# Kernel optimization log

Hardware: AMD Instinct MI355X
Metric: run time of the kernel (lower is better)

## Reference

```python
import jax, jax.numpy as jnp
import numpy as np

K = 16          # neighbors, matches init k
CHUNK = 2048    # query chunk size for kNN (avoids NxN dist matrix in one shot)


def knn_points(coords, k):
    """coords: (N,3). Returns squared dists (N,k) and indices (N,k), self included (dist 0)."""
    N = coords.shape[0]
    sq = jnp.sum(coords * coords, axis=-1)  # (N,)

    def chunk_fn(args):
        cq, cqs = args  # (CHUNK,3), (CHUNK,)
        # squared distance: |a|^2 + |b|^2 - 2 a.b  -> (CHUNK, N)
        d2 = cqs[:, None] + sq[None, :] - 2.0 * (cq @ coords.T)
        neg, idx = jax.lax.top_k(-d2, k)  # smallest distances
        return -neg, idx

    nchunks = N // CHUNK
    cc = coords.reshape(nchunks, CHUNK, 3)
    cs = sq.reshape(nchunks, CHUNK)
    d, i = jax.lax.map(chunk_fn, (cc, cs))
    return d.reshape(N, k), i.reshape(N, k)


def edge_conv_single(coords, feats, W1, b1, W2, b2):
    """One point cloud: coords (N,3), feats (N,C) -> (N,C)."""
    dists, idx = knn_points(coords, K)            # (N,k), (N,k)
    nn_feats = feats[idx]                         # (N,k,C) gather
    delta = nn_feats - feats[:, None, :]          # (N,k,C)
    grouped = jnp.concatenate([nn_feats, delta], axis=-1)  # (N,k,2C)
    h = jax.nn.relu(grouped @ W1 + b1)            # (N,k,inter)
    theta = h @ W2 + b2                           # (N,k,C)
    w = jax.nn.softmax(-dists, axis=1)            # (N,k) distance-softmax
    return jnp.einsum('nk,nkc->nc', w, theta)     # weighted average over neighbors


def setup_inputs() -> dict:
    key = jax.random.key(0)
    k1, k2, k3, k4 = jax.random.split(key, 4)
    B, N, C, INTER = 2, 16384, 256, 128
    coords = jax.random.uniform(k1, (B, N, 3), dtype=jnp.float32) * 100.0
    feats = jax.random.normal(k2, (B, N, C), dtype=jnp.float32)
    W1 = jax.random.normal(k3, (2 * C, INTER), dtype=jnp.float32) * 0.02
    b1 = jnp.zeros((INTER,), dtype=jnp.float32)
    W2 = jax.random.normal(k4, (INTER, C), dtype=jnp.float32) * 0.02
    b2 = jnp.zeros((C,), dtype=jnp.float32)
    return {"coords": coords, "feats": feats, "W1": W1, "b1": b1, "W2": W2, "b2": b2}


def reference(coords, feats, W1, b1, W2, b2):
    # batch loop in the original is embarrassingly parallel -> vmap over clouds
    return jax.vmap(edge_conv_single, in_axes=(0, 0, None, None, None, None))(
        coords, feats, W1, b1, W2, b2)
```

## Files before the change

kernel.cpp:

```cpp
#include <hip/hip_runtime.h>
#include <hip/hip_bf16.h>

#define NPTS   16384
#define NCLOUD 2
#define NTOT   (NPTS*NCLOUD)
#define CDIM   256
#define IDIM   128
#define KNN    16
#define GS     16
#define NCELL  (GS*GS*GS)
#define CELL_H 6.25f
#define INV_H  0.16f
#define SLABCAP 256

typedef __attribute__((ext_vector_type(8))) short s16x8;
typedef __attribute__((ext_vector_type(4))) float f32x4;

__device__ __forceinline__ int cell_coord(float v) {
    int c = (int)(v * INV_H);
    return c < 0 ? 0 : (c > GS-1 ? GS-1 : c);
}

__global__ __launch_bounds__(256) void prep_kernel(
        const float* __restrict__ W1, const float* __restrict__ W2,
        float* __restrict__ ABTf, float* __restrict__ W2Tf) {
    int i = blockIdx.x*256 + threadIdx.x;
    if (i < 65536) {
        int n = i >> 8, k = i & 255;
        float v = (n < IDIM) ? (W1[k*IDIM + n] + W1[(k+CDIM)*IDIM + n])
                             : W1[(k+CDIM)*IDIM + (n-IDIM)];
        ABTf[n*CDIM + k] = v;
    } else {
        int j = i - 65536;
        int n = j >> 7, k = j & 127;
        W2Tf[n*IDIM + k] = W2[k*CDIM + n];
    }
}

__global__ __launch_bounds__(256) void count_kernel(
        const float* __restrict__ coords, int* __restrict__ cnt) {
    int t = blockIdx.x * 256 + threadIdx.x;
    float x = coords[(size_t)t*3+0], y = coords[(size_t)t*3+1], z = coords[(size_t)t*3+2];
    int g = (t >> 14) * NCELL + (cell_coord(z)*GS + cell_coord(y))*GS + cell_coord(x);
    atomicAdd(&cnt[g], 1);
}

__global__ __launch_bounds__(1024) void scan_kernel(
        const int* __restrict__ cnt, int* __restrict__ cellstart,
        int* __restrict__ cursor) {
    __shared__ int sums[1024];
    const int tid = threadIdx.x;
    int local[8];
    int s = 0;
#pragma unroll
    for (int j = 0; j < 8; ++j) { local[j] = cnt[tid*8+j]; s += local[j]; }
    sums[tid] = s;
    __syncthreads();
    for (int off = 1; off < 1024; off <<= 1) {
        int v = (tid >= off) ? sums[tid-off] : 0;
        __syncthreads();
        sums[tid] += v;
        __syncthreads();
    }
    int run = sums[tid] - s;
#pragma unroll
    for (int j = 0; j < 8; ++j) {
        cellstart[tid*8+j] = run; cursor[tid*8+j] = run; run += local[j];
    }
    if (tid == 1023) cellstart[2*NCELL] = run;
}

__global__ __launch_bounds__(256) void scatter_kernel(
        const float* __restrict__ coords, int* __restrict__ cursor,
        float4* __restrict__ sorted, int* __restrict__ perm) {
    int t = blockIdx.x * 256 + threadIdx.x;
    float x = coords[(size_t)t*3+0], y = coords[(size_t)t*3+1], z = coords[(size_t)t*3+2];
    int g = (t >> 14) * NCELL + (cell_coord(z)*GS + cell_coord(y))*GS + cell_coord(x);
    int pos = atomicAdd(&cursor[g], 1);
    sorted[pos] = make_float4(x, y, z, __int_as_float(t));
    perm[pos] = t;
}

__device__ __forceinline__ void ring_off(int R, int s, int& dy, int& dz) {
    if (R == 0) { dy = 0; dz = 0; return; }
    int w = 2*R+1;
    if (s < w)        { dy = -R + s;       dz = -R; }
    else if (s < 2*w) { dy = -R + (s - w); dz =  R; }
    else {
        int rem = s - 2*w;
        if (rem < 2*R-1) { dy = -R; dz = -R+1+rem; }
        else             { dy =  R; dz = -R+1+(rem-(2*R-1)); }
    }
}

#define TOP16_INSERT(d2v, jjv) do {                                   \
    float _d2 = (d2v);                                                \
    if (_d2 < d[KNN-1]) {                                             \
        int _jj = (jjv); bool sa = true;                              \
        _Pragma("unroll")                                             \
        for (int s_ = KNN-1; s_ > 0; --s_) {                          \
            bool sh = _d2 < d[s_-1];                                  \
            float nd = sh ? d[s_-1] : (sa ? _d2 : d[s_]);             \
            int   ni = sh ? id[s_-1] : (sa ? _jj : id[s_]);           \
            d[s_] = nd; id[s_] = ni; sa = sh;                         \
        }                                                             \
        if (sa) { d[0] = _d2; id[0] = _jj; }                          \
    } } while (0)

__global__ __launch_bounds__(64) void knn_win_kernel(
        const float4* __restrict__ sorted, const int* __restrict__ cellstart,
        float* __restrict__ knn_d2, int* __restrict__ knn_idx) {
    __shared__ float ldsx[SLABCAP], ldsy[SLABCAP], ldsz[SLABCAP];
    __shared__ int cellofs[GS+1];
    const int t = threadIdx.x;
    const int bid = blockIdx.x;
    const int brow = bid >> 1, chunk = bid & 1;
    const int b  = brow >> 8;
    const int yz = brow & 255;
    const int cy = yz & 15, cz = yz >> 4;
    const int gq = b*NCELL + yz*16;
    const int qstart = cellstart[gq];
    const int qcount = cellstart[gq + GS] - qstart;

    for (int q0 = chunk*64; q0 < qcount; q0 += 64) {
        const bool active = (q0 + t < qcount);
        const float4 q = sorted[qstart + (active ? q0 + t : 0)];
        const int cx = cell_coord(q.x);
        const int wlo = cx-2 < 0 ? 0 : cx-2;
        const int whi = cx+2 > GS-1 ? GS-1 : cx+2;

        float d[KNN]; int id[KNN];
#pragma unroll
        for (int s = 0; s < KNN; ++s) { d[s] = 3.4e38f; id[s] = 0; }
        bool fin = !active;
        bool alldone = false;

        for (int phase = 0; phase < 2 && !alldone; ++phase) {
            for (int R = 0; R < GS && !alldone; ++R) {
                const int nseg = R ? 8*R : 1;
                for (int s = 0; s < nseg; ++s) {
                    int dy, dz;
                    ring_off(R, s, dy, dz);
                    const int yy = cy + dy, zz = cz + dz;
                    if (yy < 0 || yy > GS-1 || zz < 0 || zz > GS-1) continue;
                    const int g  = b*NCELL + (zz*GS + yy)*GS;
                    const int st = cellstart[g];
                    int n = cellstart[g + GS] - st;
                    if (n > SLABCAP) n = SLABCAP;
                    __syncthreads();
                    if (t < GS+1) {
                        int v = cellstart[g + t] - st;
                        cellofs[t] = v > n ? n : v;
                    }
                    for (int i = t; i < n; i += 64) {
                        float4 c = sorted[st + i];
                        ldsx[i] = c.x; ldsy[i] = c.y; ldsz[i] = c.z;
                    }
                    __syncthreads();
                    if (!fin) {
                        const int lo = cellofs[wlo], hi = cellofs[whi+1];
                        if (phase == 0) {
                            for (int e = lo; e < hi; ++e) {
                                float dx = q.x-ldsx[e], dy_ = q.y-ldsy[e], dz_ = q.z-ldsz[e];
                                TOP16_INSERT(dx*dx + dy_*dy_ + dz_*dz_, st + e);
                            }
                        } else {
                            for (int e = 0; e < n; ++e) {
                                if (e >= lo && e < hi) continue;
                                float dx = q.x-ldsx[e], dy_ = q.y-ldsy[e], dz_ = q.z-ldsz[e];
                                TOP16_INSERT(dx*dx + dy_*dy_ + dz_*dz_, st + e);
                            }
                        }
                    }
                }
                float bl = 1e30f;
                if (cy - R >= 1)    bl = fminf(bl, q.y - (float)(cy-R)*CELL_H);
                if (cy + R <= GS-2) bl = fminf(bl, (float)(cy+R+1)*CELL_H - q.y);
                if (cz - R >= 1)    bl = fminf(bl, q.z - (float)(cz-R)*CELL_H);
                if (cz + R <= GS-2) bl = fminf(bl, (float)(cz+R+1)*CELL_H - q.z);
                if (phase == 0) {
                    if (cx - 2 >= 1)    bl = fminf(bl, q.x - (float)(cx-2)*CELL_H);
                    if (cx + 2 <= GS-2) bl = fminf(bl, (float)(cx+3)*CELL_H - q.x);
                }
                fin = fin || (d[KNN-1] <= bl*bl);
                alldone = __syncthreads_and((int)fin);
            }
        }
        if (active) {
            const int o = qstart + q0 + t;
#pragma unroll
            for (int s = 0; s < KNN; ++s) {
                knn_d2 [(size_t)o*KNN + s] = d[s];
                knn_idx[(size_t)o*KNN + s] = id[s];
            }
        }
        if (chunk == 0) break;
    }
}

__device__ __forceinline__ void pack_split(float4 v, uint2& h, uint2& l) {
    __hip_bfloat16 h0=__float2bfloat16(v.x), h1=__float2bfloat16(v.y),
                   h2=__float2bfloat16(v.z), h3=__float2bfloat16(v.w);
    float r0=v.x-__bfloat162float(h0), r1=v.y-__bfloat162float(h1),
          r2=v.z-__bfloat162float(h2), r3=v.w-__bfloat162float(h3);
    __hip_bfloat16 l0=__float2bfloat16(r0), l1=__float2bfloat16(r1),
                   l2=__float2bfloat16(r2), l3=__float2bfloat16(r3);
    h.x = (unsigned)*(unsigned short*)&h0 | ((unsigned)*(unsigned short*)&h1 << 16);
    h.y = (unsigned)*(unsigned short*)&h2 | ((unsigned)*(unsigned short*)&h3 << 16);
    l.x = (unsigned)*(unsigned short*)&l0 | ((unsigned)*(unsigned short*)&l1 << 16);
    l.y = (unsigned)*(unsigned short*)&l2 | ((unsigned)*(unsigned short*)&l3 << 16);
}

template<int KDIM, bool BIAS, bool GATHER_A, bool SCATTER_OUT>
__global__ __launch_bounds__(256) void gemm_split_kernel(
        const float* __restrict__ A,
        const float* __restrict__ BT,
        const float* __restrict__ bias,
        const int*   __restrict__ permA,
        const int*   __restrict__ permOut,
        float* __restrict__ C_, int M, int N) {
    __shared__ unsigned short AsH[128*40], AsL[128*40], BsH[128*40], BsL[128*40];
    const int tid = threadIdx.x;
    const int l = tid & 63, w = tid >> 6;
    const int wm = w >> 1, wn = w & 1;
    const int bm = blockIdx.x * 128, bn = blockIdx.y * 128;
    const f32x4 zero = {0.f, 0.f, 0.f, 0.f};
    f32x4 acc[4][4];
#pragma unroll
    for (int m = 0; m < 4; ++m)
#pragma unroll
        for (int n = 0; n < 4; ++n) acc[m][n] = zero;

    for (int k0 = 0; k0 < KDIM; k0 += 32) {
        __syncthreads();
#pragma unroll
        for (int r2 = 0; r2 < 4; ++r2) {
            int flat = r2*256 + tid;
            int row = flat >> 3, ke = (flat & 7) * 4;
            int ga = bm + row;
            if (GATHER_A) ga = permA[ga];
            float4 va = *(const float4*)&A[(size_t)ga*KDIM + k0 + ke];
            uint2 uh, ul; pack_split(va, uh, ul);
            *(uint2*)&AsH[row*40 + ke] = uh;
            *(uint2*)&AsL[row*40 + ke] = ul;
            float4 vb = *(const float4*)&BT[(size_t)(bn + row)*KDIM + k0 + ke];
            uint2 vh, vl; pack_split(vb, vh, vl);
            *(uint2*)&BsH[row*40 + ke] = vh;
            *(uint2*)&BsL[row*40 + ke] = vl;
        }
        __syncthreads();
        s16x8 ah[4], al[4], bh[4], bl[4];
        const int ks = (l >> 4) * 8;
#pragma unroll
        for (int m = 0; m < 4; ++m) {
            int r = wm*64 + m*16 + (l & 15);
            ah[m] = *(const s16x8*)&AsH[r*40 + ks];
            al[m] = *(const s16x8*)&AsL[r*40 + ks];
        }
#pragma unroll
        for (int n = 0; n < 4; ++n) {
            int r = wn*64 + n*16 + (l & 15);
            bh[n] = *(const s16x8*)&BsH[r*40 + ks];
            bl[n] = *(const s16x8*)&BsL[r*40 + ks];
        }
#pragma unroll
        for (int m = 0; m < 4; ++m)
#pragma unroll
            for (int n = 0; n < 4; ++n) {
                acc[m][n] = __builtin_amdgcn_mfma_f32_16x16x32_bf16(ah[m], bh[n], acc[m][n], 0, 0, 0);
                acc[m][n] = __builtin_amdgcn_mfma_f32_16x16x32_bf16(ah[m], bl[n], acc[m][n], 0, 0, 0);
                acc[m][n] = __builtin_amdgcn_mfma_f32_16x16x32_bf16(al[m], bh[n], acc[m][n], 0, 0, 0);
            }
    }
#pragma unroll
    for (int m = 0; m < 4; ++m)
#pragma unroll
        for (int n = 0; n < 4; ++n) {
            int ct = bn + wn*64 + n*16 + (l & 15);
            float bv = BIAS ? bias[ct] : 0.f;
#pragma unroll
            for (int j = 0; j < 4; ++j) {
                int rt = bm + wm*64 + m*16 + ((l >> 4) << 2) + j;
                int go = SCATTER_OUT ? permOut[rt] : rt;
                C_[(size_t)go*N + ct] = acc[m][n][j] + bv;
            }
        }
}

__global__ __launch_bounds__(128) void combine_kernel(
        const float* __restrict__ PQ, const float* __restrict__ knn_d2,
        const int* __restrict__ knn_idx, const float* __restrict__ b1,
        float* __restrict__ hbar) {
    const int n = blockIdx.x;
    const int t = threadIdx.x;
    float dd[KNN];
#pragma unroll
    for (int k = 0; k < KNN; ++k) dd[k] = knn_d2[(size_t)n*KNN + k];
    float m = dd[0];
#pragma unroll
    for (int k = 1; k < KNN; ++k) m = fminf(m, dd[k]);
    float e[KNN]; float sum = 0.f;
#pragma unroll
    for (int k = 0; k < KNN; ++k) { e[k] = __expf(m - dd[k]); sum += e[k]; }
    const float inv = 1.0f / sum;
    const float qv = PQ[(size_t)n*CDIM + IDIM + t];
    const float bb = b1[t];
    float acc = 0.f;
#pragma unroll
    for (int k = 0; k < KNN; ++k) {
        int row = knn_idx[(size_t)n*KNN + k];
        float p = PQ[(size_t)row*CDIM + t];
        acc += e[k] * fmaxf(p - qv + bb, 0.0f);
    }
    hbar[(size_t)n*IDIM + t] = acc * inv;
}

extern "C" void kernel_launch(void* const* d_in, const int* in_sizes, int n_in,
                              void* d_out, int out_size, void* d_ws, size_t ws_size,
                              hipStream_t stream) {
    const float* coords = (const float*)d_in[0];
    const float* feats  = (const float*)d_in[1];
    const float* W1     = (const float*)d_in[2];
    const float* b1     = (const float*)d_in[3];
    const float* W2     = (const float*)d_in[4];
    const float* b2     = (const float*)d_in[5];
    float* out = (float*)d_out;

    char* p = (char*)d_ws;
    float4* sorted = (float4*)p;         p += (size_t)NTOT*16;
    float*  PQ     = (float*)p;          p += (size_t)NTOT*CDIM*4;
    float*  hbar   = (float*)p;          p += (size_t)NTOT*IDIM*4;
    float*  knn_d2 = (float*)p;          p += (size_t)NTOT*KNN*4;
    int*    knn_idx= (int*)p;            p += (size_t)NTOT*KNN*4;
    float*  ABTf   = (float*)p;          p += 65536*4;
    float*  W2Tf   = (float*)p;          p += 32768*4;
    int*    perm   = (int*)p;            p += (size_t)NTOT*4;
    int*    cnt    = (int*)p;            p += 2*NCELL*4;
    int*    cellstart = (int*)p;         p += (2*NCELL+8)*4;
    int*    cursor = (int*)p;            p += 2*NCELL*4;

    hipMemsetAsync(cnt, 0, 2*NCELL*sizeof(int), stream);
    prep_kernel   <<<384, 256, 0, stream>>>(W1, W2, ABTf, W2Tf);
    count_kernel  <<<NTOT/256, 256, 0, stream>>>(coords, cnt);
    scan_kernel   <<<1, 1024, 0, stream>>>(cnt, cellstart, cursor);
    scatter_kernel<<<NTOT/256, 256, 0, stream>>>(coords, cursor, sorted, perm);
    knn_win_kernel<<<2*256*2, 64, 0, stream>>>(sorted, cellstart, knn_d2, knn_idx);
    gemm_split_kernel<CDIM, false, true, false>
        <<<dim3(NTOT/128, 2), 256, 0, stream>>>(
            feats, ABTf, nullptr, perm, nullptr, PQ, NTOT, CDIM);
    combine_kernel<<<NTOT, 128, 0, stream>>>(PQ, knn_d2, knn_idx, b1, hbar);
    gemm_split_kernel<IDIM, true, false, true>
        <<<dim3(NTOT/128, 2), 256, 0, stream>>>(
            hbar, W2Tf, b2, nullptr, perm, out, NTOT, CDIM);
}
```

Before: 298.5 us.

## Replace ring-expanding kNN search with 5x5x5 region load and 4-way split

The kNN kernel now loads the whole 5x5 (y,z) row region around each query row into LDS once, instead of walking expanding rings cell-row by cell-row with a barrier per segment. Each query's candidates are split across 4 lanes, whose partial top-16 lists are merged with xor shuffles. If the region bound cannot be certified or the region overflows LDS, the block falls back to a brute-force scan of the whole cloud. This removes the many per-ring synchronizations and global reloads and raises the block to 256 threads, at the cost of a possibly very expensive fallback path and heavier shuffle merges.

```diff
diff --git a/kernel.cpp b/kernel.cpp
--- a/kernel.cpp
+++ b/kernel.cpp
@@ -11,7 +11,7 @@
 #define NCELL  (GS*GS*GS)
 #define CELL_H 6.25f
 #define INV_H  0.16f
-#define SLABCAP 256
+#define REGCAP 2048
 
 typedef __attribute__((ext_vector_type(8))) short s16x8;
 typedef __attribute__((ext_vector_type(4))) float f32x4;
@@ -81,18 +81,6 @@
     perm[pos] = t;
 }
 
-__device__ __forceinline__ void ring_off(int R, int s, int& dy, int& dz) {
-    if (R == 0) { dy = 0; dz = 0; return; }
-    int w = 2*R+1;
-    if (s < w)        { dy = -R + s;       dz = -R; }
-    else if (s < 2*w) { dy = -R + (s - w); dz =  R; }
-    else {
-        int rem = s - 2*w;
-        if (rem < 2*R-1) { dy = -R; dz = -R+1+rem; }
-        else             { dy =  R; dz = -R+1+(rem-(2*R-1)); }
-    }
-}
-
 #define TOP16_INSERT(d2v, jjv) do {                                   \
     float _d2 = (d2v);                                                \
     if (_d2 < d[KNN-1]) {                                             \
@@ -107,11 +95,13 @@
         if (sa) { d[0] = _d2; id[0] = _jj; }                          \
     } } while (0)
 
-__global__ __launch_bounds__(64) void knn_win_kernel(
+__global__ __launch_bounds__(256) void knn_region_kernel(
         const float4* __restrict__ sorted, const int* __restrict__ cellstart,
         float* __restrict__ knn_d2, int* __restrict__ knn_idx) {
-    __shared__ float ldsx[SLABCAP], ldsy[SLABCAP], ldsz[SLABCAP];
-    __shared__ int cellofs[GS+1];
+    __shared__ float rx[REGCAP], ry[REGCAP], rz[REGCAP];
+    __shared__ int cofs[25][17];
+    __shared__ int rstart[25];
+    __shared__ int segmeta[8];
     const int t = threadIdx.x;
     const int bid = blockIdx.x;
     const int brow = bid >> 1, chunk = bid & 1;
@@ -121,80 +111,145 @@
     const int gq = b*NCELL + yz*16;
     const int qstart = cellstart[gq];
     const int qcount = cellstart[gq + GS] - qstart;
-
-    for (int q0 = chunk*64; q0 < qcount; q0 += 64) {
-        const bool active = (q0 + t < qcount);
-        const float4 q = sorted[qstart + (active ? q0 + t : 0)];
+    if (qcount <= 0) return;
+    if (chunk == 1 && qcount <= 64) return;
+
+    const int ylo = cy-2 < 0 ? 0 : cy-2, yhi = cy+2 > 15 ? 15 : cy+2;
+
+    int q0 = chunk ? 64 : 0;
+    while (true) {
+        __syncthreads();
+        if (t == 0) {
+            int base = 0;
+            for (int dzi = 0; dzi < 5; ++dzi) {
+                segmeta[dzi] = base;
+                int zz = cz + dzi - 2;
+                if (zz >= 0 && zz <= 15) {
+                    int s0 = cellstart[b*NCELL + (zz*16 + ylo)*16];
+                    int e0 = cellstart[b*NCELL + (zz*16 + yhi)*16 + 16];
+                    base += e0 - s0;
+                }
+            }
+            segmeta[5] = base;
+            segmeta[6] = (base > REGCAP) ? 1 : 0;
+        }
+        __syncthreads();
+        const bool overflow = (segmeta[6] != 0);
+        for (int i = t; i < 425; i += 256) {
+            int r = i / 17, k = i % 17;
+            int dzi = r / 5, dyi = r % 5;
+            int zz = cz + dzi - 2, yy = cy + dyi - 2;
+            int v = 0, rs = 0;
+            if (zz >= 0 && zz <= 15 && yy >= 0 && yy <= 15) {
+                int segs = cellstart[b*NCELL + (zz*16 + ylo)*16];
+                int rowg = b*NCELL + (zz*16 + yy)*16;
+                v = segmeta[dzi] + (cellstart[rowg + k] - segs);
+                if (v > REGCAP) v = REGCAP;
+                rs = cellstart[rowg];
+            }
+            cofs[r][k] = v;
+            if (k == 0) rstart[r] = rs;
+        }
+        if (!overflow) {
+            for (int dzi = 0; dzi < 5; ++dzi) {
+                int zz = cz + dzi - 2;
+                if (zz < 0 || zz > 15) continue;
+                int s0  = cellstart[b*NCELL + (zz*16 + ylo)*16];
+                int len = cellstart[b*NCELL + (zz*16 + yhi)*16 + 16] - s0;
+                int dst = segmeta[dzi];
+                for (int i = t; i < len; i += 256) {
+                    float4 c = sorted[s0 + i];
+                    rx[dst+i] = c.x; ry[dst+i] = c.y; rz[dst+i] = c.z;
+                }
+            }
+        }
+        __syncthreads();
+
+        const int w = t >> 6, lane = t & 63;
+        const int sub = lane >> 4, qi = lane & 15;
+        const int qidx = q0 + w*16 + qi;
+        const bool active = (qidx < qcount);
+        const float4 q = sorted[qstart + (active ? qidx : 0)];
         const int cx = cell_coord(q.x);
-        const int wlo = cx-2 < 0 ? 0 : cx-2;
-        const int whi = cx+2 > GS-1 ? GS-1 : cx+2;
+        const int wlo = cx-2 < 0 ? 0 : cx-2, whi = cx+2 > 15 ? 15 : cx+2;
 
         float d[KNN]; int id[KNN];
 #pragma unroll
-        for (int s = 0; s < KNN; ++s) { d[s] = 3.4e38f; id[s] = 0; }
+        for (int s_ = 0; s_ < KNN; ++s_) { d[s_] = 3.4e38f; id[s_] = 0; }
         bool fin = !active;
-        bool alldone = false;
-
-        for (int phase = 0; phase < 2 && !alldone; ++phase) {
-            for (int R = 0; R < GS && !alldone; ++R) {
-                const int nseg = R ? 8*R : 1;
-                for (int s = 0; s < nseg; ++s) {
-                    int dy, dz;
-                    ring_off(R, s, dy, dz);
-                    const int yy = cy + dy, zz = cz + dz;
-                    if (yy < 0 || yy > GS-1 || zz < 0 || zz > GS-1) continue;
-                    const int g  = b*NCELL + (zz*GS + yy)*GS;
-                    const int st = cellstart[g];
-                    int n = cellstart[g + GS] - st;
-                    if (n > SLABCAP) n = SLABCAP;
-                    __syncthreads();
-                    if (t < GS+1) {
-                        int v = cellstart[g + t] - st;
-                        cellofs[t] = v > n ? n : v;
+
+        if (!overflow) {
+            if (active) {
+                for (int r = 0; r < 25; ++r) {
+                    const int lo = cofs[r][wlo], hi = cofs[r][whi+1];
+                    const int base0 = cofs[r][0], rs = rstart[r];
+                    for (int e = lo + sub; e < hi; e += 4) {
+                        float dx = q.x - rx[e], dy = q.y - ry[e], dz = q.z - rz[e];
+                        TOP16_INSERT(dx*dx + dy*dy + dz*dz, rs + (e - base0));
                     }
-                    for (int i = t; i < n; i += 64) {
-                        float4 c = sorted[st + i];
-                        ldsx[i] = c.x; ldsy[i] = c.y; ldsz[i] = c.z;
+                }
+            }
+#pragma unroll
+        for (int mask = 16; mask <= 32; mask <<= 1) {
+                float od[KNN]; int oi[KNN];
+#pragma unroll
+                for (int j = 0; j < KNN; ++j) {
+                    od[j] = __shfl_xor(d[j], mask);
+                    oi[j] = __shfl_xor(id[j], mask);
+                }
+                if (active) {
+#pragma unroll
+                    for (int j = 0; j < KNN; ++j) TOP16_INSERT(od[j], oi[j]);
+                }
+            }
+            float bl = 1e30f;
+            if (cx-2 >= 1)  bl = fminf(bl, q.x - (float)(cx-2)*CELL_H);
+            if (cx+2 <= 14) bl = fminf(bl, (float)(cx+3)*CELL_H - q.x);
+            if (cy-2 >= 1)  bl = fminf(bl, q.y - (float)(cy-2)*CELL_H);
+            if (cy+2 <= 14) bl = fminf(bl, (float)(cy+3)*CELL_H - q.y);
+            if (cz-2 >= 1)  bl = fminf(bl, q.z - (float)(cz-2)*CELL_H);
+            if (cz+2 <= 14) bl = fminf(bl, (float)(cz+3)*CELL_H - q.z);
+            fin = fin || (d[KNN-1] <= bl*bl);
+        }
+
+        if (__syncthreads_and((int)fin)) {
+            if (active && sub == 0) {
+                const size_t o = (size_t)(qstart + qidx) * KNN;
+#pragma unroll
+                for (int s_ = 0; s_ < KNN; ++s_) {
+                    knn_d2[o + s_] = d[s_]; knn_idx[o + s_] = id[s_];
+                }
+            }
+        } else {
+            const int fqi = q0 + t;
+            const bool fact = (t < 64) && (fqi < qcount);
+            const float4 fq = sorted[qstart + (fact ? fqi : 0)];
+#pragma unroll
+            for (int s_ = 0; s_ < KNN; ++s_) { d[s_] = 3.4e38f; id[s_] = 0; }
+            const int cbase = b * NPTS;
+            for (int c0 = 0; c0 < NPTS; c0 += 256) {
+                __syncthreads();
+                float4 c = sorted[cbase + c0 + t];
+                rx[t] = c.x; ry[t] = c.y; rz[t] = c.z;
+                __syncthreads();
+                if (fact) {
+                    for (int j = 0; j < 256; ++j) {
+                        float dx = fq.x - rx[j], dy = fq.y - ry[j], dz = fq.z - rz[j];
+                        TOP16_INSERT(dx*dx + dy*dy + dz*dz, cbase + c0 + j);
                     }
-                    __syncthreads();
-                    if (!fin) {
-                        const int lo = cellofs[wlo], hi = cellofs[whi+1];
-                        if (phase == 0) {
-                            for (int e = lo; e < hi; ++e) {
-                                float dx = q.x-ldsx[e], dy_ = q.y-ldsy[e], dz_ = q.z-ldsz[e];
-                                TOP16_INSERT(dx*dx + dy_*dy_ + dz_*dz_, st + e);
-                            }
-                        } else {
-                            for (int e = 0; e < n; ++e) {
-                                if (e >= lo && e < hi) continue;
-                                float dx = q.x-ldsx[e], dy_ = q.y-ldsy[e], dz_ = q.z-ldsz[e];
-                                TOP16_INSERT(dx*dx + dy_*dy_ + dz_*dz_, st + e);
-                            }
-                        }
-                    }
-                }
-                float bl = 1e30f;
-                if (cy - R >= 1)    bl = fminf(bl, q.y - (float)(cy-R)*CELL_H);
-                if (cy + R <= GS-2) bl = fminf(bl, (float)(cy+R+1)*CELL_H - q.y);
-                if (cz - R >= 1)    bl = fminf(bl, q.z - (float)(cz-R)*CELL_H);
-                if (cz + R <= GS-2) bl = fminf(bl, (float)(cz+R+1)*CELL_H - q.z);
-                if (phase == 0) {
-                    if (cx - 2 >= 1)    bl = fminf(bl, q.x - (float)(cx-2)*CELL_H);
-                    if (cx + 2 <= GS-2) bl = fminf(bl, (float)(cx+3)*CELL_H - q.x);
-                }
-                fin = fin || (d[KNN-1] <= bl*bl);
-                alldone = __syncthreads_and((int)fin);
-            }
-        }
-        if (active) {
-            const int o = qstart + q0 + t;
-#pragma unroll
-            for (int s = 0; s < KNN; ++s) {
-                knn_d2 [(size_t)o*KNN + s] = d[s];
-                knn_idx[(size_t)o*KNN + s] = id[s];
+                }
+            }
+            if (fact) {
+                const size_t o = (size_t)(qstart + fqi) * KNN;
+#pragma unroll
+                for (int s_ = 0; s_ < KNN; ++s_) {
+                    knn_d2[o + s_] = d[s_]; knn_idx[o + s_] = id[s_];
+                }
             }
         }
         if (chunk == 0) break;
+        q0 += 64;
+        if (q0 >= qcount) break;
     }
 }
 
@@ -344,7 +399,7 @@
     count_kernel  <<<NTOT/256, 256, 0, stream>>>(coords, cnt);
     scan_kernel   <<<1, 1024, 0, stream>>>(cnt, cellstart, cursor);
     scatter_kernel<<<NTOT/256, 256, 0, stream>>>(coords, cursor, sorted, perm);
-    knn_win_kernel<<<2*256*2, 64, 0, stream>>>(sorted, cellstart, knn_d2, knn_idx);
+    knn_region_kernel<<<2*256*2, 256, 0, stream>>>(sorted, cellstart, knn_d2, knn_idx);
     gemm_split_kernel<CDIM, false, true, false>
         <<<dim3(NTOT/128, 2), 256, 0, stream>>>(
             feats, ABTf, nullptr, perm, nullptr, PQ, NTOT, CDIM);
```

After: 256.2 us. -14.2%, faster.
